# Optimization experiments

Hardware: AMD Instinct MI355X
Metric: run time of the kernel (lower is better)

## Reference

```python
import jax, jax.numpy as jnp
import numpy as np
import math

NB_BASIS = 100          # add_gaussian_basis_functions
SEQ_SIDE = 14           # 14x14 = 196 image feature grid
RIDGE = 0.5             # ridge_penalty for G = F^T (F F^T + lam I)^-1
BASIS_VAR = 0.001       # sigma = 0.001 * I for every basis Gaussian
TWO_PI = 2.0 * math.pi
EPS_COV = 1e-6          # stabilizer added to fitted covariance


def _positions():
    # compute_positions_efficient: linspace(shift, 1-shift, L0) meshgrid, L0=L1=14
    s = 1.0 / SEQ_SIDE
    lin = np.linspace(s, 1.0 - s, SEQ_SIDE)
    px, py = np.meshgrid(lin, lin, indexing='ij')
    return jnp.asarray(np.stack([px.ravel(), py.ravel()], axis=-1), jnp.float32)  # [L,2]


def _basis_mus():
    # add_gaussian_basis_functions: 10x10 grid of means over [0,1]^2
    lin = np.linspace(0.0, 1.0, int(math.sqrt(NB_BASIS)))
    mx, my = np.meshgrid(lin, lin, indexing='ij')
    return jnp.asarray(np.stack([mx.ravel(), my.ravel()], axis=-1), jnp.float32)  # [N,2]


def _G_matrix(pos, mus):
    # F[j, i] = N(pos_i ; mu_j, BASIS_VAR * I)  (isotropic 2D Gaussian density)
    d2 = jnp.sum((pos[None, :, :] - mus[:, None, :]) ** 2, axis=-1)       # [N,L]
    F = jnp.exp(-0.5 * d2 / BASIS_VAR) / (TWO_PI * BASIS_VAR)
    A = F @ F.T + RIDGE * jnp.eye(NB_BASIS, dtype=F.dtype)                # [N,N]
    return F.T @ jnp.linalg.inv(A)                                        # [L,N]


def setup_inputs() -> dict:
    key = jax.random.key(0)
    ks = jax.random.split(key, 7)
    B, L, H, M, GL, O = 256, 196, 1024, 512, 1, 2048
    x = jax.random.normal(ks[0], (B, L, H), jnp.float32)
    x_mask = jnp.zeros((B, L), dtype=bool)  # True = padded position
    W1 = jax.random.normal(ks[1], (H, M), jnp.float32) * 0.02
    b1 = jnp.zeros((M,), jnp.float32)
    W2 = jax.random.normal(ks[2], (M, GL), jnp.float32) * 0.02
    b2 = jnp.zeros((GL,), jnp.float32)
    Wm = jax.random.normal(ks[3], (H * GL, O), jnp.float32) * 0.02
    bm = jnp.zeros((O,), jnp.float32)
    return {"x": x, "x_mask": x_mask, "W1": W1, "b1": b1,
            "W2": W2, "b2": b2, "Wm": Wm, "bm": bm}


def reference(x, x_mask, W1, b1, W2, b2, Wm, bm):
    # x: [B,L,H] grid features, x_mask: [B,L] bool padding mask
    pos = _positions()            # [L,2]
    mus = _basis_mus()            # [N,2]
    G = _G_matrix(pos, mus)       # [L,N] shared across batch (single length bucket)

    # --- MLP attention (glimpses=1), softmax over sequence dim ---
    logits = jax.nn.relu(x @ W1 + b1) @ W2 + b2          # [B,L,1]
    logits = jnp.where(x_mask[..., None], -1e9, logits)
    att = jax.nn.softmax(logits, axis=1)                 # [B,L,1]
    p = att[..., 0]                                      # [B,L]

    # --- fit 2D Gaussian to attention over positions (continuous softmax params) ---
    mu = p @ pos                                         # [B,2]
    d = pos[None, :, :] - mu[:, None, :]                 # [B,L,2]
    Sigma = jnp.einsum('bl,bli,blj->bij', p, d, d) + EPS_COV * jnp.eye(2, dtype=x.dtype)

    # --- r_j = E_{N(mu,Sigma)}[psi_j] = N(mu_j ; mu, Sigma + BASIS_VAR*I) ---
    S = Sigma + BASIS_VAR * jnp.eye(2, dtype=x.dtype)    # [B,2,2]
    a, b_, c, ddg = S[:, 0, 0], S[:, 0, 1], S[:, 1, 0], S[:, 1, 1]
    det = a * ddg - b_ * c                               # [B]
    Sinv = jnp.stack([jnp.stack([ddg, -b_], -1),
                      jnp.stack([-c, a], -1)], -2) / det[:, None, None]
    dm = mu[:, None, :] - mus[None, :, :]                # [B,N,2]
    quad = jnp.einsum('bni,bij,bnj->bn', dm, Sinv, dm)
    r = jnp.exp(-0.5 * quad) / (TWO_PI * jnp.sqrt(det)[:, None])  # [B,N]

    # --- value_function: B = V^T G; context = B r ---
    Bmat = jnp.einsum('bld,ln->bdn', x, G)               # [B,H,N]
    ctx = jnp.einsum('bdn,bn->bd', Bmat, r)              # [B,H]

    return ctx @ Wm + bm                                 # [B,FLAT_OUT_SIZE]
```

## Files before the change

kernel.cpp:

```cpp
#include <hip/hip_runtime.h>

typedef _Float16 half8v __attribute__((ext_vector_type(8)));
typedef float    f32x4  __attribute__((ext_vector_type(4)));
typedef unsigned short ushort_t;

__device__ __forceinline__ unsigned short f2h(float f) {
  _Float16 h = (_Float16)f;
  return __builtin_bit_cast(unsigned short, h);
}
__device__ __forceinline__ unsigned f2h2(float lo, float hi) {
  return (unsigned)f2h(lo) | ((unsigned)f2h(hi) << 16);
}
__device__ __forceinline__ float lin14(int i) {
  double s = 1.0 / 14.0, stop = 1.0 - s;
  double step = (stop - s) / 13.0;
  return (float)((i == 13) ? stop : s + i * step);
}
__device__ __forceinline__ float lin10(int i) {
  double st = 1.0 / 9.0;
  return (float)((i == 9) ? 1.0 : i * st);
}
__device__ __forceinline__ float wave_sum(float v) {
  #pragma unroll
  for (int o = 32; o; o >>= 1) v += __shfl_xor(v, o, 64);
  return v;
}
__device__ __forceinline__ float wave_max(float v) {
  #pragma unroll
  for (int o = 32; o; o >>= 1) v = fmaxf(v, __shfl_xor(v, o, 64));
  return v;
}
__device__ __forceinline__ float blk_sum(float v, float* red) {
  v = wave_sum(v);
  if ((threadIdx.x & 63) == 0) red[threadIdx.x >> 6] = v;
  __syncthreads();
  v = red[0] + red[1] + red[2] + red[3];
  __syncthreads();
  return v;
}
__device__ __forceinline__ float blk_max(float v, float* red) {
  v = wave_max(v);
  if ((threadIdx.x & 63) == 0) red[threadIdx.x >> 6] = v;
  __syncthreads();
  v = fmaxf(fmaxf(red[0], red[1]), fmaxf(red[2], red[3]));
  __syncthreads();
  return v;
}

__global__ void k_F(float* __restrict__ posg, float* __restrict__ musg,
                    float* __restrict__ Fg) {
  int idx = blockIdx.x * 256 + threadIdx.x;
  if (idx < 196) { posg[2*idx] = lin14(idx / 14); posg[2*idx+1] = lin14(idx % 14); }
  if (idx < 100) { musg[2*idx] = lin10(idx / 10); musg[2*idx+1] = lin10(idx % 10); }
  if (idx < 19600) {
    int k = idx / 196, l = idx % 196;
    float mx = lin10(k / 10), my = lin10(k % 10);
    float px = lin14(l / 14), py = lin14(l % 14);
    double dx = (double)mx - (double)px, dy = (double)my - (double)py;
    double d2 = dx * dx + dy * dy;
    Fg[idx] = (float)(exp(-500.0 * d2) / (6.283185307179586 * 0.001));
  }
}

__global__ void k_A(const float* __restrict__ Fg, double* __restrict__ A) {
  int i = blockIdx.x, j = threadIdx.x;
  if (j < 100) {
    const float* Fi = Fg + i * 196;
    const float* Fj = Fg + j * 196;
    double s = 0.0;
    for (int l = 0; l < 196; ++l) s += (double)Fi[l] * (double)Fj[l];
    if (i == j) s += 0.5;
    A[i * 100 + j] = s;
  }
}

__global__ __launch_bounds__(256) void k_inv(const double* __restrict__ Ag,
                                             double* __restrict__ Ainv) {
  __shared__ double rowraw[100], colraw[100], rkv[100], ckv[100];
  int t = threadIdx.x;
  int rb = t / 10, cb = t % 10;
  bool own = t < 250;
  double a[4][10];
  if (own) {
    #pragma unroll
    for (int r = 0; r < 4; ++r)
      #pragma unroll
      for (int c = 0; c < 10; ++c)
        a[r][c] = Ag[(4 * rb + r) * 100 + 10 * cb + c];
  }
  __syncthreads();
  for (int k = 0; k < 100; ++k) {
    int krb = k >> 2, klr = k & 3;
    int kcb = k / 10, klc = k - 10 * kcb;
    if (own && rb == krb) {
      #pragma unroll
      for (int r = 0; r < 4; ++r)
        if (r == klr) {
          #pragma unroll
          for (int c = 0; c < 10; ++c) rowraw[10 * cb + c] = a[r][c];
        }
    }
    if (own && cb == kcb) {
      #pragma unroll
      for (int c = 0; c < 10; ++c)
        if (c == klc) {
          #pragma unroll
          for (int r = 0; r < 4; ++r) colraw[4 * rb + r] = a[r][c];
        }
    }
    __syncthreads();
    if (t < 100) {
      double p = rowraw[k], pinv = 1.0 / p;
      rkv[t] = (t == k) ? 1.0 + pinv : rowraw[t] * pinv;
      ckv[t] = (t == k) ? p - 1.0    : colraw[t];
    }
    __syncthreads();
    if (own) {
      double ckl[4], rkl[10];
      #pragma unroll
      for (int r = 0; r < 4; ++r) ckl[r] = ckv[4 * rb + r];
      #pragma unroll
      for (int c = 0; c < 10; ++c) rkl[c] = rkv[10 * cb + c];
      #pragma unroll
      for (int r = 0; r < 4; ++r)
        #pragma unroll
        for (int c = 0; c < 10; ++c)
          a[r][c] = fma(-ckl[r], rkl[c], a[r][c]);
    }
  }
  if (own) {
    #pragma unroll
    for (int r = 0; r < 4; ++r)
      #pragma unroll
      for (int c = 0; c < 10; ++c)
        Ainv[(4 * rb + r) * 100 + 10 * cb + c] = a[r][c];
  }
}

__global__ void k_G(const float* __restrict__ Fg, const double* __restrict__ Ainv,
                    float* __restrict__ Gt) {
  int l = blockIdx.x, n = threadIdx.x;
  if (n < 100) {
    double s = 0.0;
    for (int k = 0; k < 100; ++k) s += (double)Fg[k * 196 + l] * Ainv[k * 100 + n];
    Gt[n * 196 + l] = (float)s;
  }
}

__global__ void k_splitw1(const float* __restrict__ W1, ushort_t* __restrict__ W1t) {
  __shared__ float t[32][33];
  int n0 = blockIdx.x * 32, k0 = blockIdx.y * 32;
  int tx = threadIdx.x, ty = threadIdx.y;
  #pragma unroll
  for (int i = 0; i < 32; i += 8)
    t[ty + i][tx] = W1[(size_t)(k0 + ty + i) * 512 + n0 + tx];
  __syncthreads();
  #pragma unroll
  for (int i = 0; i < 32; i += 8)
    W1t[(size_t)(n0 + ty + i) * 1024 + k0 + tx] = f2h(t[tx][ty + i]);
}

__global__ void k_wmT(const float* __restrict__ Wm, ushort_t* __restrict__ WmT) {
  __shared__ float t[32][33];
  int n0 = blockIdx.x * 32, k0 = blockIdx.y * 32;
  int tx = threadIdx.x, ty = threadIdx.y;
  #pragma unroll
  for (int i = 0; i < 32; i += 8)
    t[ty + i][tx] = Wm[(size_t)(k0 + ty + i) * 2048 + n0 + tx];
  __syncthreads();
  #pragma unroll
  for (int i = 0; i < 32; i += 8)
    WmT[(size_t)(n0 + ty + i) * 1024 + k0 + tx] = f2h(t[tx][ty + i]);
}

__global__ __launch_bounds__(256, 2) void k_gemm1(
    const float* __restrict__ x, const ushort_t* __restrict__ W1t,
    const float* __restrict__ b1, const float* __restrict__ W2,
    float* __restrict__ logits) {
  __shared__ __align__(16) ushort_t As[2][128 * 40];
  __shared__ __align__(16) ushort_t Bs[2][128 * 40];

  int bid  = blockIdx.x;
  int bid2 = (bid & 7) * 196 + (bid >> 3);
  int tm = bid2 >> 2, tn = bid2 & 3;
  size_t row0 = (size_t)tm * 128;
  int n0 = tn * 128;
  int tid = threadIdx.x, lane = tid & 63;
  int wid = tid >> 6, wm = wid >> 1, wn = wid & 1;

  const float*    xp = x   + (row0 + (tid >> 2)) * 1024 + ((tid & 3) << 3);
  const ushort_t* wp = W1t + (size_t)(n0 + (tid >> 2)) * 1024 + ((tid & 3) << 3);
  int so = (tid >> 2) * 40 + ((tid & 3) << 3);

  int aro = (wm * 64 + (lane & 15)) * 40 + ((lane >> 4) << 3);
  int bro = (wn * 64 + (lane & 15)) * 40 + ((lane >> 4) << 3);

  f32x4 acc[4][4] = {};

  float4 aP[4], aQ[4]; uint4 bP[2], bQ[2];

  auto issueP = [&](int ks) {
    #pragma unroll
    for (int r = 0; r < 2; ++r) {
      aP[2*r]   = *(const float4*)(xp + ks * 32 + r * 64 * 1024);
      aP[2*r+1] = *(const float4*)(xp + ks * 32 + r * 64 * 1024 + 4);
      bP[r]     = *(const uint4*)(wp + ks * 32 + r * 64 * 1024);
    }
  };
  auto issueQ = [&](int ks) {
    #pragma unroll
    for (int r = 0; r < 2; ++r) {
      aQ[2*r]   = *(const float4*)(xp + ks * 32 + r * 64 * 1024);
      aQ[2*r+1] = *(const float4*)(xp + ks * 32 + r * 64 * 1024 + 4);
      bQ[r]     = *(const uint4*)(wp + ks * 32 + r * 64 * 1024);
    }
  };
  auto writeP = [&](int buf) {
    #pragma unroll
    for (int r = 0; r < 2; ++r) {
      uint4 w;
      w.x = f2h2(aP[2*r].x, aP[2*r].y);   w.y = f2h2(aP[2*r].z, aP[2*r].w);
      w.z = f2h2(aP[2*r+1].x, aP[2*r+1].y); w.w = f2h2(aP[2*r+1].z, aP[2*r+1].w);
      *(uint4*)&As[buf][so + r * 64 * 40] = w;
      *(uint4*)&Bs[buf][so + r * 64 * 40] = bP[r];
    }
  };
  auto writeQ = [&](int buf) {
    #pragma unroll
    for (int r = 0; r < 2; ++r) {
      uint4 w;
      w.x = f2h2(aQ[2*r].x, aQ[2*r].y);   w.y = f2h2(aQ[2*r].z, aQ[2*r].w);
      w.z = f2h2(aQ[2*r+1].x, aQ[2*r+1].y); w.w = f2h2(aQ[2*r+1].z, aQ[2*r+1].w);
      *(uint4*)&As[buf][so + r * 64 * 40] = w;
      *(uint4*)&Bs[buf][so + r * 64 * 40] = bQ[r];
    }
  };
  auto mmac = [&](int buf) {
    half8v af[4], bf[4];
    #pragma unroll
    for (int i = 0; i < 4; ++i) af[i] = *(const half8v*)&As[buf][aro + i * 16 * 40];
    #pragma unroll
    for (int i = 0; i < 4; ++i) bf[i] = *(const half8v*)&Bs[buf][bro + i * 16 * 40];
    #pragma unroll
    for (int i = 0; i < 4; ++i)
      #pragma unroll
      for (int j = 0; j < 4; ++j)
        acc[i][j] = __builtin_amdgcn_mfma_f32_16x16x32_f16(af[i], bf[j], acc[i][j], 0, 0, 0);
  };

  issueP(0);
  writeP(0);
  issueQ(1);
  __syncthreads();

  #pragma unroll 1
  for (int kp = 0; kp < 16; ++kp) {
    int e = 2 * kp;
    if (e < 30) issueP(e + 2);
    mmac(0);
    if (e < 31) writeQ(1);
    __syncthreads();
    if (e + 1 < 30) issueQ(e + 3);
    mmac(1);
    if (e + 1 < 31) writeP(0);
    __syncthreads();
  }

  int cbase = n0 + wn * 64 + (lane & 15);
  float b1v[4], w2v[4];
  #pragma unroll
  for (int j = 0; j < 4; ++j) { b1v[j] = b1[cbase + j * 16]; w2v[j] = W2[cbase + j * 16]; }
  float part[4][4];
  #pragma unroll
  for (int i = 0; i < 4; ++i)
    #pragma unroll
    for (int q = 0; q < 4; ++q) {
      float s = 0.f;
      #pragma unroll
      for (int j = 0; j < 4; ++j) {
        float h = acc[i][j][q] + b1v[j];
        s += fmaxf(h, 0.f) * w2v[j];
      }
      part[i][q] = s;
    }
  #pragma unroll
  for (int off = 1; off < 16; off <<= 1)
    #pragma unroll
    for (int i = 0; i < 4; ++i)
      #pragma unroll
      for (int q = 0; q < 4; ++q)
        part[i][q] += __shfl_xor(part[i][q], off, 64);
  if ((lane & 15) == 0) {
    int rbase = (int)row0 + wm * 64 + ((lane >> 4) << 2);
    #pragma unroll
    for (int i = 0; i < 4; ++i)
      #pragma unroll
      for (int q = 0; q < 4; ++q)
        atomicAdd(&logits[rbase + i * 16 + q], part[i][q]);
  }
}

__global__ __launch_bounds__(256) void k_batch(
    const float* __restrict__ logits, const unsigned char* __restrict__ mask,
    const float* __restrict__ b2, const float* __restrict__ pos,
    const float* __restrict__ mus, const float* __restrict__ Gt,
    float* __restrict__ g_out) {
  __shared__ float red[4];
  __shared__ float rsh[100];
  int b = blockIdx.x, tid = threadIdx.x;
  bool act = tid < 196;
  float lg = -1e30f;
  if (act) {
    lg = logits[b * 196 + tid] + b2[0];
    if (mask[b * 196 + tid]) lg = -1e9f;
  }
  float m = blk_max(lg, red);
  float e = act ? expf(lg - m) : 0.f;
  float Z = blk_sum(e, red);
  float pv = e / Z;
  float px = act ? pos[2 * tid] : 0.f, py = act ? pos[2 * tid + 1] : 0.f;
  float mux = blk_sum(pv * px, red);
  float muy = blk_sum(pv * py, red);
  float dx = px - mux, dy = py - muy;
  float sxx = blk_sum(pv * dx * dx, red);
  float sxy = blk_sum(pv * dx * dy, red);
  float syy = blk_sum(pv * dy * dy, red);
  float aa = (sxx + 1e-6f) + 1e-3f;
  float bb = sxy;
  float dd = (syy + 1e-6f) + 1e-3f;
  float det = aa * dd - bb * bb;
  float scale = 1.f / (6.2831853071795864f * sqrtf(det));
  if (tid < 100) {
    float dmx = mux - mus[2 * tid], dmy = muy - mus[2 * tid + 1];
    float quad = (dd * dmx * dmx - 2.f * bb * dmx * dmy + aa * dmy * dmy) / det;
    rsh[tid] = expf(-0.5f * quad) * scale;
  }
  __syncthreads();
  if (act) {
    float s = 0.f;
    #pragma unroll 4
    for (int n = 0; n < 100; ++n) s = fmaf(Gt[n * 196 + tid], rsh[n], s);
    g_out[b * 196 + tid] = s;
  }
}

__global__ __launch_bounds__(256) void k_ctx(const float* __restrict__ x,
                                             const float* __restrict__ g,
                                             ushort_t* __restrict__ ctxh) {
  int b = blockIdx.y, seg = blockIdx.x, tid = threadIdx.x;
  __shared__ float gs[196];
  if (tid < 196) gs[tid] = g[b * 196 + tid];
  __syncthreads();
  int d = seg * 256 + tid;
  const float* xp = x + (size_t)b * 200704 + d;
  float acc = 0.f;
  #pragma unroll 8
  for (int l = 0; l < 196; ++l) acc = fmaf(xp[(size_t)l * 1024], gs[l], acc);
  ctxh[b * 1024 + d] = f2h(acc);
}

__global__ __launch_bounds__(256, 2) void k_out2(
    const ushort_t* __restrict__ ctxh, const ushort_t* __restrict__ WmT,
    const float* __restrict__ bm, float* __restrict__ out) {
  __shared__ __align__(16) ushort_t As[2][64 * 40];
  __shared__ __align__(16) ushort_t Bs[2][128 * 40];
  int n0 = blockIdx.x * 128;
  int m0 = blockIdx.y * 64;
  int tid = threadIdx.x, lane = tid & 63;
  int wid = tid >> 6, wm = wid >> 1, wn = wid & 1;

  int arow = tid >> 2, aseg = (tid & 3) << 3;
  const ushort_t* ap = ctxh + (m0 + arow) * 1024 + aseg;
  int aso = arow * 40 + aseg;
  int brow = tid >> 1, bsh = (tid & 1) << 4;
  const ushort_t* bp = WmT + (size_t)(n0 + brow) * 1024 + bsh;
  int bso = brow * 40 + bsh;

  int aro = (wm * 32 + (lane & 15)) * 40 + ((lane >> 4) << 3);
  int bro = (wn * 64 + (lane & 15)) * 40 + ((lane >> 4) << 3);

  f32x4 acc[2][4] = {};
  uint4 a4, b4[2];
  a4 = *(const uint4*)ap;
  b4[0] = *(const uint4*)bp; b4[1] = *(const uint4*)(bp + 8);
  *(uint4*)&As[0][aso] = a4;
  *(uint4*)&Bs[0][bso] = b4[0]; *(uint4*)&Bs[0][bso + 8] = b4[1];
  __syncthreads();

  int cur = 0;
  for (int ks = 0; ks < 32; ++ks) {
    if (ks < 31) {
      a4 = *(const uint4*)(ap + (ks + 1) * 32);
      b4[0] = *(const uint4*)(bp + (ks + 1) * 32);
      b4[1] = *(const uint4*)(bp + (ks + 1) * 32 + 8);
    }
    half8v af[2], bf[4];
    #pragma unroll
    for (int i = 0; i < 2; ++i) af[i] = *(const half8v*)&As[cur][aro + i * 16 * 40];
    #pragma unroll
    for (int j = 0; j < 4; ++j) bf[j] = *(const half8v*)&Bs[cur][bro + j * 16 * 40];
    #pragma unroll
    for (int i = 0; i < 2; ++i)
      #pragma unroll
      for (int j = 0; j < 4; ++j)
        acc[i][j] = __builtin_amdgcn_mfma_f32_16x16x32_f16(af[i], bf[j], acc[i][j], 0, 0, 0);
    if (ks < 31) {
      *(uint4*)&As[cur ^ 1][aso] = a4;
      *(uint4*)&Bs[cur ^ 1][bso] = b4[0]; *(uint4*)&Bs[cur ^ 1][bso + 8] = b4[1];
    }
    __syncthreads();
    cur ^= 1;
  }

  int rbase = m0 + wm * 32 + ((lane >> 4) << 2);
  int cbase = n0 + wn * 64 + (lane & 15);
  #pragma unroll
  for (int j = 0; j < 4; ++j) {
    float bmv = bm[cbase + j * 16];
    #pragma unroll
    for (int i = 0; i < 2; ++i)
      #pragma unroll
      for (int q = 0; q < 4; ++q)
        out[(size_t)(rbase + i * 16 + q) * 2048 + cbase + j * 16] = acc[i][j][q] + bmv;
  }
}

extern "C" void kernel_launch(void* const* d_in, const int* in_sizes, int n_in,
                              void* d_out, int out_size, void* d_ws, size_t ws_size,
                              hipStream_t stream) {
  const float* x  = (const float*)d_in[0];
  const unsigned char* xmask = (const unsigned char*)d_in[1];
  const float* W1 = (const float*)d_in[2];
  const float* b1 = (const float*)d_in[3];
  const float* W2 = (const float*)d_in[4];
  const float* b2 = (const float*)d_in[5];
  const float* Wm = (const float*)d_in[6];
  const float* bm = (const float*)d_in[7];
  float* out = (float*)d_out;

  char* ws = (char*)d_ws;
  float*    Fg     = (float*)(ws + 0);
  double*   Ainv   = (double*)(ws + 78400);
  double*   Atmp   = (double*)(ws + 158400);
  float*    posg   = (float*)(ws + 238400);
  float*    musg   = (float*)(ws + 239968);
  float*    Gt     = (float*)(ws + 240768);
  float*    logits = (float*)(ws + 319168);
  float*    gbuf   = (float*)(ws + 519872);
  ushort_t* ctxh   = (ushort_t*)(ws + 720576);
  ushort_t* W1t    = (ushort_t*)(ws + 1244864);
  ushort_t* WmT    = (ushort_t*)(ws + 2293440);

  k_F<<<77, 256, 0, stream>>>(posg, musg, Fg);
  k_A<<<100, 128, 0, stream>>>(Fg, Atmp);
  k_inv<<<1, 256, 0, stream>>>(Atmp, Ainv);
  k_G<<<196, 128, 0, stream>>>(Fg, Ainv, Gt);
  k_splitw1<<<dim3(16, 32), dim3(32, 8), 0, stream>>>(W1, W1t);
  k_wmT<<<dim3(64, 32), dim3(32, 8), 0, stream>>>(Wm, WmT);
  hipMemsetAsync(logits, 0, 200704, stream);
  k_gemm1<<<1568, 256, 0, stream>>>(x, W1t, b1, W2, logits);
  k_batch<<<256, 256, 0, stream>>>(logits, xmask, b2, posg, musg, Gt, gbuf);
  k_ctx<<<dim3(4, 256), 256, 0, stream>>>(x, gbuf, ctxh);
  k_out2<<<dim3(16, 4), 256, 0, stream>>>(ctxh, WmT, bm, out);
}
```

Before: 623.4 us.

## Deepen gemm1 K-tile to 128, vectorize ctx reduction, merge weight transposes

The main GEMM now stages a 128-wide K slice per iteration in a single LDS buffer, using register prefetch of the next slice, instead of 32-wide double-buffered slices. That gives 8 outer iterations instead of 32 and fewer barriers per unit of MFMA work. The ctx reduction now has one block per batch with float4 loads and four accumulators per thread, and the two weight-transpose kernels are merged into one launch. The larger LDS footprint (about 68KB) and many more live prefetch registers (64 floats plus 32 dwords) may lower occupancy below the launch bound of 2, and k_ctx now launches only 256 blocks.

```diff
diff --git a/kernel.cpp b/kernel.cpp
--- a/kernel.cpp
+++ b/kernel.cpp
@@ -147,38 +147,31 @@
   }
 }
 
-__global__ void k_splitw1(const float* __restrict__ W1, ushort_t* __restrict__ W1t) {
+__global__ void k_tr(const float* __restrict__ W1, ushort_t* __restrict__ W1t,
+                     const float* __restrict__ Wm, ushort_t* __restrict__ WmT) {
   __shared__ float t[32][33];
+  int z = blockIdx.z;
+  if (z == 0 && blockIdx.x >= 16) return;
+  const float* src = z ? Wm : W1;
+  ushort_t* dst    = z ? WmT : W1t;
+  int NCOL = z ? 2048 : 512;
   int n0 = blockIdx.x * 32, k0 = blockIdx.y * 32;
   int tx = threadIdx.x, ty = threadIdx.y;
   #pragma unroll
   for (int i = 0; i < 32; i += 8)
-    t[ty + i][tx] = W1[(size_t)(k0 + ty + i) * 512 + n0 + tx];
+    t[ty + i][tx] = src[(size_t)(k0 + ty + i) * NCOL + n0 + tx];
   __syncthreads();
   #pragma unroll
   for (int i = 0; i < 32; i += 8)
-    W1t[(size_t)(n0 + ty + i) * 1024 + k0 + tx] = f2h(t[tx][ty + i]);
-}
-
-__global__ void k_wmT(const float* __restrict__ Wm, ushort_t* __restrict__ WmT) {
-  __shared__ float t[32][33];
-  int n0 = blockIdx.x * 32, k0 = blockIdx.y * 32;
-  int tx = threadIdx.x, ty = threadIdx.y;
-  #pragma unroll
-  for (int i = 0; i < 32; i += 8)
-    t[ty + i][tx] = Wm[(size_t)(k0 + ty + i) * 2048 + n0 + tx];
-  __syncthreads();
-  #pragma unroll
-  for (int i = 0; i < 32; i += 8)
-    WmT[(size_t)(n0 + ty + i) * 1024 + k0 + tx] = f2h(t[tx][ty + i]);
+    dst[(size_t)(n0 + ty + i) * 1024 + k0 + tx] = f2h(t[tx][ty + i]);
 }
 
 __global__ __launch_bounds__(256, 2) void k_gemm1(
     const float* __restrict__ x, const ushort_t* __restrict__ W1t,
     const float* __restrict__ b1, const float* __restrict__ W2,
     float* __restrict__ logits) {
-  __shared__ __align__(16) ushort_t As[2][128 * 40];
-  __shared__ __align__(16) ushort_t Bs[2][128 * 40];
+  __shared__ __align__(16) ushort_t As[128 * 136];
+  __shared__ __align__(16) ushort_t Bs[128 * 136];
 
   int bid  = blockIdx.x;
   int bid2 = (bid & 7) * 196 + (bid >> 3);
@@ -188,83 +181,71 @@
   int tid = threadIdx.x, lane = tid & 63;
   int wid = tid >> 6, wm = wid >> 1, wn = wid & 1;
 
-  const float*    xp = x   + (row0 + (tid >> 2)) * 1024 + ((tid & 3) << 3);
-  const ushort_t* wp = W1t + (size_t)(n0 + (tid >> 2)) * 1024 + ((tid & 3) << 3);
-  int so = (tid >> 2) * 40 + ((tid & 3) << 3);
-
-  int aro = (wm * 64 + (lane & 15)) * 40 + ((lane >> 4) << 3);
-  int bro = (wn * 64 + (lane & 15)) * 40 + ((lane >> 4) << 3);
+  const float* xq = x + (row0 + (tid >> 3)) * 1024 + ((tid & 7) << 2);
+  int soa = (tid >> 3) * 136 + ((tid & 7) << 2);
+  const ushort_t* wq = W1t + (size_t)(n0 + (tid >> 4)) * 1024 + ((tid & 15) << 3);
+  int sob = (tid >> 4) * 136 + ((tid & 15) << 3);
+
+  int aro = (wm * 64 + (lane & 15)) * 136 + ((lane >> 4) << 3);
+  int bro = (wn * 64 + (lane & 15)) * 136 + ((lane >> 4) << 3);
 
   f32x4 acc[4][4] = {};
-
-  float4 aP[4], aQ[4]; uint4 bP[2], bQ[2];
-
-  auto issueP = [&](int ks) {
-    #pragma unroll
-    for (int r = 0; r < 2; ++r) {
-      aP[2*r]   = *(const float4*)(xp + ks * 32 + r * 64 * 1024);
-      aP[2*r+1] = *(const float4*)(xp + ks * 32 + r * 64 * 1024 + 4);
-      bP[r]     = *(const uint4*)(wp + ks * 32 + r * 64 * 1024);
-    }
-  };
-  auto issueQ = [&](int ks) {
-    #pragma unroll
-    for (int r = 0; r < 2; ++r) {
-      aQ[2*r]   = *(const float4*)(xp + ks * 32 + r * 64 * 1024);
-      aQ[2*r+1] = *(const float4*)(xp + ks * 32 + r * 64 * 1024 + 4);
-      bQ[r]     = *(const uint4*)(wp + ks * 32 + r * 64 * 1024);
-    }
-  };
-  auto writeP = [&](int buf) {
-    #pragma unroll
-    for (int r = 0; r < 2; ++r) {
-      uint4 w;
-      w.x = f2h2(aP[2*r].x, aP[2*r].y);   w.y = f2h2(aP[2*r].z, aP[2*r].w);
-      w.z = f2h2(aP[2*r+1].x, aP[2*r+1].y); w.w = f2h2(aP[2*r+1].z, aP[2*r+1].w);
-      *(uint4*)&As[buf][so + r * 64 * 40] = w;
-      *(uint4*)&Bs[buf][so + r * 64 * 40] = bP[r];
-    }
-  };
-  auto writeQ = [&](int buf) {
-    #pragma unroll
-    for (int r = 0; r < 2; ++r) {
-      uint4 w;
-      w.x = f2h2(aQ[2*r].x, aQ[2*r].y);   w.y = f2h2(aQ[2*r].z, aQ[2*r].w);
-      w.z = f2h2(aQ[2*r+1].x, aQ[2*r+1].y); w.w = f2h2(aQ[2*r+1].z, aQ[2*r+1].w);
-      *(uint4*)&As[buf][so + r * 64 * 40] = w;
-      *(uint4*)&Bs[buf][so + r * 64 * 40] = bQ[r];
-    }
-  };
-  auto mmac = [&](int buf) {
-    half8v af[4], bf[4];
-    #pragma unroll
-    for (int i = 0; i < 4; ++i) af[i] = *(const half8v*)&As[buf][aro + i * 16 * 40];
-    #pragma unroll
-    for (int i = 0; i < 4; ++i) bf[i] = *(const half8v*)&Bs[buf][bro + i * 16 * 40];
-    #pragma unroll
-    for (int i = 0; i < 4; ++i)
-      #pragma unroll
-      for (int j = 0; j < 4; ++j)
-        acc[i][j] = __builtin_amdgcn_mfma_f32_16x16x32_f16(af[i], bf[j], acc[i][j], 0, 0, 0);
-  };
-
-  issueP(0);
-  writeP(0);
-  issueQ(1);
-  __syncthreads();
-
+  float4 ax[4][4];
+  uint4  bw[8];
+
+#define G1_ISSUE(kc)                                                          \
+  do {                                                                        \
+    _Pragma("unroll") for (int p = 0; p < 4; ++p)                             \
+      _Pragma("unroll") for (int j = 0; j < 4; ++j)                           \
+        ax[p][j] = *(const float4*)(xq + (kc) * 128 + p * 32 * 1024 + j * 32);\
+    _Pragma("unroll") for (int p = 0; p < 8; ++p)                             \
+      bw[p] = *(const uint4*)(wq + (kc) * 128 + p * 16 * 1024);               \
+  } while (0)
+
+#define G1_WRITE()                                                            \
+  do {                                                                        \
+    _Pragma("unroll") for (int p = 0; p < 4; ++p)                             \
+      _Pragma("unroll") for (int j = 0; j < 4; ++j) {                         \
+        uint2 w2_;                                                            \
+        w2_.x = f2h2(ax[p][j].x, ax[p][j].y);                                 \
+        w2_.y = f2h2(ax[p][j].z, ax[p][j].w);                                 \
+        *(uint2*)&As[soa + p * 32 * 136 + j * 32] = w2_;                      \
+      }                                                                       \
+    _Pragma("unroll") for (int p = 0; p < 8; ++p)                             \
+      *(uint4*)&Bs[sob + p * 16 * 136] = bw[p];                               \
+  } while (0)
+
+#define G1_MMAC()                                                             \
+  do {                                                                        \
+    _Pragma("unroll") for (int s = 0; s < 4; ++s) {                           \
+      half8v af[4], bf[4];                                                    \
+      _Pragma("unroll") for (int i = 0; i < 4; ++i)                           \
+        af[i] = *(const half8v*)&As[aro + i * 16 * 136 + s * 32];             \
+      _Pragma("unroll") for (int i = 0; i < 4; ++i)                           \
+        bf[i] = *(const half8v*)&Bs[bro + i * 16 * 136 + s * 32];             \
+      _Pragma("unroll") for (int i = 0; i < 4; ++i)                           \
+        _Pragma("unroll") for (int j = 0; j < 4; ++j)                         \
+          acc[i][j] = __builtin_amdgcn_mfma_f32_16x16x32_f16(                 \
+              af[i], bf[j], acc[i][j], 0, 0, 0);                              \
+    }                                                                         \
+  } while (0)
+
+  G1_ISSUE(0);
+  G1_WRITE();
+  __syncthreads();
   #pragma unroll 1
-  for (int kp = 0; kp < 16; ++kp) {
-    int e = 2 * kp;
-    if (e < 30) issueP(e + 2);
-    mmac(0);
-    if (e < 31) writeQ(1);
+  for (int kc = 1; kc < 8; ++kc) {
+    G1_ISSUE(kc);
+    G1_MMAC();
     __syncthreads();
-    if (e + 1 < 30) issueQ(e + 3);
-    mmac(1);
-    if (e + 1 < 31) writeP(0);
+    G1_WRITE();
     __syncthreads();
   }
+  G1_MMAC();
+
+#undef G1_ISSUE
+#undef G1_WRITE
+#undef G1_MMAC
 
   int cbase = n0 + wn * 64 + (lane & 15);
   float b1v[4], w2v[4];
@@ -347,16 +328,22 @@
 __global__ __launch_bounds__(256) void k_ctx(const float* __restrict__ x,
                                              const float* __restrict__ g,
                                              ushort_t* __restrict__ ctxh) {
-  int b = blockIdx.y, seg = blockIdx.x, tid = threadIdx.x;
+  int b = blockIdx.x, tid = threadIdx.x;
   __shared__ float gs[196];
   if (tid < 196) gs[tid] = g[b * 196 + tid];
   __syncthreads();
-  int d = seg * 256 + tid;
+  int d = tid << 2;
   const float* xp = x + (size_t)b * 200704 + d;
-  float acc = 0.f;
-  #pragma unroll 8
-  for (int l = 0; l < 196; ++l) acc = fmaf(xp[(size_t)l * 1024], gs[l], acc);
-  ctxh[b * 1024 + d] = f2h(acc);
+  float a0 = 0.f, a1 = 0.f, a2 = 0.f, a3 = 0.f;
+  #pragma unroll 4
+  for (int l = 0; l < 196; ++l) {
+    float4 v = *(const float4*)(xp + (size_t)l * 1024);
+    float gl = gs[l];
+    a0 = fmaf(v.x, gl, a0); a1 = fmaf(v.y, gl, a1);
+    a2 = fmaf(v.z, gl, a2); a3 = fmaf(v.w, gl, a3);
+  }
+  uint2 o; o.x = f2h2(a0, a1); o.y = f2h2(a2, a3);
+  *(uint2*)&ctxh[(size_t)b * 1024 + d] = o;
 }
 
 __global__ __launch_bounds__(256, 2) void k_out2(
@@ -455,11 +442,10 @@
   k_A<<<100, 128, 0, stream>>>(Fg, Atmp);
   k_inv<<<1, 256, 0, stream>>>(Atmp, Ainv);
   k_G<<<196, 128, 0, stream>>>(Fg, Ainv, Gt);
-  k_splitw1<<<dim3(16, 32), dim3(32, 8), 0, stream>>>(W1, W1t);
-  k_wmT<<<dim3(64, 32), dim3(32, 8), 0, stream>>>(Wm, WmT);
+  k_tr<<<dim3(64, 32, 2), dim3(32, 8), 0, stream>>>(W1, W1t, Wm, WmT);
   hipMemsetAsync(logits, 0, 200704, stream);
   k_gemm1<<<1568, 256, 0, stream>>>(x, W1t, b1, W2, logits);
   k_batch<<<256, 256, 0, stream>>>(logits, xmask, b2, posg, musg, Gt, gbuf);
-  k_ctx<<<dim3(4, 256), 256, 0, stream>>>(x, gbuf, ctxh);
+  k_ctx<<<256, 256, 0, stream>>>(x, gbuf, ctxh);
   k_out2<<<dim3(16, 4), 256, 0, stream>>>(ctxh, WmT, bm, out);
 }
```

Result: no change. 620.8 us (-0.4%).
